# Kernel tuning notes

Hardware: AMD Instinct MI355X
Metric: run time of the kernel (lower is better)

Reference implementation:

```python
import jax, jax.numpy as jnp
import numpy as np

B, S, E, H, NF, NH, NIT = 64, 1024, 1024, 2048, 8, 4, 10
TEMP, XNOISE, LR = 1.0, 0.1, 0.1

PNAMES = ['ce_w1','ce_b1','ce_g','ce_be','ce_w2','ce_b2',
          'tp_w1','tp_b1','tp_g','tp_be','tp_w2','tp_b2',
          'en_w1','en_b1','en_g','en_be','en_w2','en_b2','en_w3','en_b3',
          'rn_w1','rn_b1','rn_g','rn_be','rn_w2','rn_b2']

def _ln(x, g, b):
    m = x.mean(-1, keepdims=True)
    v = ((x - m) ** 2).mean(-1, keepdims=True)
    return (x - m) * jax.lax.rsqrt(v + 1e-5) * g + b

def setup_inputs() -> dict:
    key = jax.random.key(0)
    ks = iter(jax.random.split(key, 40))
    w = lambda shape: jax.random.normal(next(ks), shape, jnp.float32) * 0.02
    z = lambda n: jnp.zeros((n,), jnp.float32)
    o = lambda n: jnp.ones((n,), jnp.float32)
    return {
        'current_embeddings': jax.random.normal(next(ks), (B, S, E), jnp.float32),
        'future_true': jax.random.normal(next(ks), (B, NF, E), jnp.float32),
        'ce_w1': w((E, H)), 'ce_b1': z(H), 'ce_g': o(H), 'ce_be': z(H), 'ce_w2': w((H, H)), 'ce_b2': z(H),
        'tp_w1': w((H, H)), 'tp_b1': z(H), 'tp_g': o(H), 'tp_be': z(H), 'tp_w2': w((H, E * NF)), 'tp_b2': z(E * NF),
        'en_w1': w((2 * E, H)), 'en_b1': z(H), 'en_g': o(H), 'en_be': z(H),
        'en_w2': w((H, H // 2)), 'en_b2': z(H // 2), 'en_w3': w((H // 2, 1)), 'en_b3': z(1),
        'rn_w1': w((3 * E, H)), 'rn_b1': z(H), 'rn_g': o(H), 'rn_be': z(H), 'rn_w2': w((H, E)), 'rn_b2': z(E),
    }

def _energy(emb, ce, ftrue, p):
    # emb: (..., NF, E); ce: (..., E); eval-mode (no dropout). Loop over t in
    # the original is a plain sum/NF -> vectorized over the NF axis here.
    ce_b = jnp.broadcast_to(ce[..., None, :], emb.shape)
    x = jnp.concatenate([emb, ce_b], axis=-1)            # (..., NF, 2E)
    x = jax.nn.relu(_ln(x @ p['en_w1'] + p['en_b1'], p['en_g'], p['en_be']))
    x = jax.nn.relu(x @ p['en_w2'] + p['en_b2'])
    coherence = (x @ p['en_w3'] + p['en_b3'])[..., 0].mean(-1)
    diffs = emb[..., 1:, :] - emb[..., :-1, :]
    smoothness = jnp.sqrt((diffs ** 2).sum(-1)).mean(-1)
    supervision = ((emb - ftrue) ** 2).mean((-1, -2))
    return coherence + 0.1 * smoothness + supervision

def _forward(cur, ft, p):
    ctx = cur.mean(1)                                    # (B, E)
    h = jax.nn.relu(_ln(ctx @ p['ce_w1'] + p['ce_b1'], p['ce_g'], p['ce_be']))
    ctx_h = h @ p['ce_w2'] + p['ce_b2']                  # (B, H)
    t = jax.nn.relu(_ln(ctx_h @ p['tp_w1'] + p['tp_b1'], p['tp_g'], p['tp_be']))
    traj = (t @ p['tp_w2'] + p['tp_b2']).reshape(B, 1, NF, E)
    # n_hypotheses identical deterministic trajectories + exploration noise
    noise = jax.random.normal(jax.random.key(42), (B, NH, NF, E), traj.dtype) * XNOISE
    hyp = traj + noise                                   # (B, NH, NF, E)
    ctx_e = ctx_h[:, :E]                                 # context[:, :embed_dim]

    emb = hyp.reshape(B * NH, NF, E)
    ce_flat = jnp.broadcast_to(ctx_e[:, None, :], (B, NH, E)).reshape(B * NH, E)
    ce_tiled = jnp.broadcast_to(ce_flat[:, None, :], (B * NH, NF, E))

    def refine(x, it):
        # all t-updates read the same snapshot of x -> fully vectorized over t
        prev = jnp.concatenate([x[:, :1], x[:, :-1]], axis=1)
        nxt = jnp.concatenate([x[:, 1:], x[:, -1:]], axis=1)
        neighbor = (prev + nxt) * 0.5
        inp = jnp.concatenate([x, ce_tiled, neighbor], axis=-1)   # (BH, NF, 3E)
        u = jax.nn.relu(_ln(inp @ p['rn_w1'] + p['rn_b1'], p['rn_g'], p['rn_be']))
        u = u @ p['rn_w2'] + p['rn_b2']
        x = x - LR * u
        ns = jax.random.normal(jax.random.fold_in(jax.random.key(7), it), x.shape, x.dtype) * (XNOISE * 0.1)
        x = jnp.where(it < NIT - 1, x + ns, x)  # noise on all but last iter
        return x, None

    emb, _ = jax.lax.scan(refine, emb, jnp.arange(NIT))
    refined = emb.reshape(B, NH, NF, E)

    ce_h = jnp.broadcast_to(ctx_e[:, None, :], (B, NH, E))
    ft_h = jnp.broadcast_to(ft[:, None], (B, NH, NF, E))
    energies = _energy(refined, ce_h, ft_h, p)           # (B, NH)
    probs = jax.nn.softmax(-energies / TEMP, axis=1)
    predictions = (refined * probs[..., None, None]).sum(1)  # (B, NF, E)
    return predictions

def reference(current_embeddings, future_true, ce_w1, ce_b1, ce_g, ce_be, ce_w2, ce_b2,
              tp_w1, tp_b1, tp_g, tp_be, tp_w2, tp_b2,
              en_w1, en_b1, en_g, en_be, en_w2, en_b2, en_w3, en_b3,
              rn_w1, rn_b1, rn_g, rn_be, rn_w2, rn_b2):
    p = dict(zip(PNAMES, (ce_w1, ce_b1, ce_g, ce_be, ce_w2, ce_b2,
                          tp_w1, tp_b1, tp_g, tp_be, tp_w2, tp_b2,
                          en_w1, en_b1, en_g, en_be, en_w2, en_b2, en_w3, en_b3,
                          rn_w1, rn_b1, rn_g, rn_be, rn_w2, rn_b2)))
    return _forward(current_embeddings, future_true, p)
```

## Files before the change

### kernel.cpp

```cpp
#include <hip/hip_runtime.h>
#include <hip/hip_bf16.h>
#include <stdint.h>

#define B_ 64
#define S_ 1024
#define E_ 1024
#define H_ 2048
#define NF_ 8
#define NH_ 4
#define NIT_ 10

typedef __attribute__((ext_vector_type(8))) short vshort8;
typedef __attribute__((ext_vector_type(8))) __bf16 vbf16x8;
typedef __attribute__((ext_vector_type(4))) float vfloat4;

typedef const __attribute__((address_space(1))) void* gas1_t;
typedef __attribute__((address_space(3))) void* las3_t;
__device__ __forceinline__ void gload16(const void* g, void* l) {
  __builtin_amdgcn_global_load_lds((gas1_t)g, (las3_t)l, 16, 0, 0);
}

__device__ __forceinline__ uint32_t rotl32(uint32_t v, int n) { return (v << n) | (v >> (32 - n)); }

__device__ __forceinline__ void threefry2x32(uint32_t k0, uint32_t k1, uint32_t x0, uint32_t x1,
                                             uint32_t& o0, uint32_t& o1) {
  uint32_t ks2 = k0 ^ k1 ^ 0x1BD11BDAu;
  x0 += k0; x1 += k1;
#define TF_R(r) { x0 += x1; x1 = rotl32(x1, (r)); x1 ^= x0; }
  TF_R(13) TF_R(15) TF_R(26) TF_R(6)
  x0 += k1;  x1 += ks2 + 1u;
  TF_R(17) TF_R(29) TF_R(16) TF_R(24)
  x0 += ks2; x1 += k0 + 2u;
  TF_R(13) TF_R(15) TF_R(26) TF_R(6)
  x0 += k0;  x1 += k1 + 3u;
  TF_R(17) TF_R(29) TF_R(16) TF_R(24)
  x0 += k1;  x1 += ks2 + 4u;
  TF_R(13) TF_R(15) TF_R(26) TF_R(6)
  x0 += ks2; x1 += k0 + 5u;
#undef TF_R
  o0 = x0; o1 = x1;
}

__device__ __forceinline__ uint32_t tf_bits_part(uint32_t k0, uint32_t k1, uint32_t i) {
  uint32_t o0, o1;
  threefry2x32(k0, k1, 0u, i, o0, o1);
  return o0 ^ o1;
}

__device__ __forceinline__ float erfinv_f(float x) {
  float w = -log1pf(-x * x);
  float p;
  if (w < 5.0f) {
    w -= 2.5f;
    p = 2.81022636e-08f;
    p = 3.43273939e-07f + p * w;
    p = -3.5233877e-06f + p * w;
    p = -4.39150654e-06f + p * w;
    p = 0.00021858087f + p * w;
    p = -0.00125372503f + p * w;
    p = -0.00417768164f + p * w;
    p = 0.246640727f + p * w;
    p = 1.50140941f + p * w;
  } else {
    w = sqrtf(w) - 3.0f;
    p = -0.000200214257f;
    p = 0.000100950558f + p * w;
    p = 0.00134934322f + p * w;
    p = -0.00367342844f + p * w;
    p = 0.00573950773f + p * w;
    p = -0.0076224613f + p * w;
    p = 0.00943887047f + p * w;
    p = 1.00167406f + p * w;
    p = 2.83297682f + p * w;
  }
  return p * x;
}

__device__ __forceinline__ float bits_to_normal(uint32_t bits) {
  uint32_t fb = (bits >> 9) | 0x3F800000u;
  float f = __uint_as_float(fb) - 1.0f;
  const float lo = -0.99999994f;
  float u = fmaxf(lo, f * 2.0f + lo);
  return 1.41421356f * erfinv_f(u);
}

__global__ __launch_bounds__(256) void colmean_partial(const float* __restrict__ cur,
                                                       float* __restrict__ part) {
  int blk = blockIdx.x;
  int b = blk >> 3, c = blk & 7;
  int t = threadIdx.x;
  const float* base = cur + ((size_t)b * S_ + (size_t)c * 128) * E_;
  float4 s = {0.f, 0.f, 0.f, 0.f};
  for (int si = 0; si < 128; ++si) {
    float4 v = *(const float4*)(base + (size_t)si * E_ + t * 4);
    s.x += v.x; s.y += v.y; s.z += v.z; s.w += v.w;
  }
  *(float4*)(part + ((size_t)c * B_ + b) * E_ + t * 4) = s;
}

__global__ __launch_bounds__(256) void colmean_final(const float* __restrict__ part,
                                                     float* __restrict__ ctx) {
  int i = blockIdx.x * 256 + threadIdx.x;
  float s = 0.f;
#pragma unroll
  for (int c = 0; c < 8; ++c) s += part[(size_t)c * (B_ * E_) + i];
  ctx[i] = s * (1.0f / S_);
}

__global__ __launch_bounds__(256) void cvt_bf16_v(const float* __restrict__ X,
                                                  __hip_bfloat16* __restrict__ Y) {
  int i = (blockIdx.x * 256 + threadIdx.x) * 8;
  float4 v0 = *(const float4*)(X + i);
  float4 v1 = *(const float4*)(X + i + 4);
  float v[8] = {v0.x, v0.y, v0.z, v0.w, v1.x, v1.y, v1.z, v1.w};
  __hip_bfloat16 o[8];
#pragma unroll
  for (int j = 0; j < 8; ++j) o[j] = __float2bfloat16(v[j]);
  *(vshort8*)&Y[i] = *(vshort8*)o;
}

__global__ __launch_bounds__(256) void transpose_to_bf16(const float* __restrict__ W,
                                                         __hip_bfloat16* __restrict__ Wt,
                                                         int K, int N, float scale) {
  __shared__ float tile[32][33];
  int n0 = blockIdx.x * 32, k0 = blockIdx.y * 32;
  int tx = threadIdx.x & 31, ty = threadIdx.x >> 5;
  for (int r = ty; r < 32; r += 8) tile[r][tx] = W[(size_t)(k0 + r) * N + n0 + tx];
  __syncthreads();
  for (int r = ty; r < 32; r += 8)
    Wt[(size_t)(n0 + r) * K + k0 + tx] = __float2bfloat16(tile[tx][r] * scale);
}

__global__ __launch_bounds__(256) void mfma_skinny(const __hip_bfloat16* __restrict__ A,
                                                   const __hip_bfloat16* __restrict__ Bt,
                                                   float* __restrict__ part,
                                                   int N, int K, int lda, int Kc) {
  __shared__ short AS[64 * 32];
  __shared__ short BS[128 * 32];
  int t = threadIdx.x;
  int lane = t & 63, wv = t >> 6;
  int n0 = blockIdx.x * 128;
  int kbeg = blockIdx.y * Kc;
  int wn = wv * 32;
  int lrow = lane & 15, kb = (lane >> 4) * 8;
  vfloat4 acc[4][2];
#pragma unroll
  for (int i = 0; i < 4; ++i)
#pragma unroll
    for (int j = 0; j < 2; ++j) acc[i][j] = (vfloat4){0.f, 0.f, 0.f, 0.f};
  const short* Ag = (const short*)A;
  const short* Bg = (const short*)Bt;
  int arow = lane >> 2;
  int acol = (lane & 3) * 8;
  for (int k0 = kbeg; k0 < kbeg + Kc; k0 += 32) {
    gload16(Ag + (size_t)(wv * 16 + arow) * lda + k0 + acol, &AS[(wv * 16) * 32]);
#pragma unroll
    for (int c = 0; c < 2; ++c)
      gload16(Bg + (size_t)(n0 + c * 64 + wv * 16 + arow) * K + k0 + acol,
              &BS[(c * 64 + wv * 16) * 32]);
    __syncthreads();
    vbf16x8 af[4], bq[2];
#pragma unroll
    for (int i = 0; i < 4; ++i) af[i] = *(const vbf16x8*)&AS[(i * 16 + lrow) * 32 + kb];
#pragma unroll
    for (int j = 0; j < 2; ++j) bq[j] = *(const vbf16x8*)&BS[(wn + j * 16 + lrow) * 32 + kb];
#pragma unroll
    for (int i = 0; i < 4; ++i)
#pragma unroll
      for (int j = 0; j < 2; ++j)
        acc[i][j] = __builtin_amdgcn_mfma_f32_16x16x32_bf16(af[i], bq[j], acc[i][j], 0, 0, 0);
    __syncthreads();
  }
  size_t zbase = (size_t)blockIdx.y * 64;
  int crow0 = (lane >> 4) * 4;
  int ccol0 = n0 + wn + lrow;
#pragma unroll
  for (int i = 0; i < 4; ++i) {
#pragma unroll
    for (int j = 0; j < 2; ++j) {
      int col = ccol0 + j * 16;
#pragma unroll
      for (int r = 0; r < 4; ++r) {
        int rowi = i * 16 + crow0 + r;
        part[(zbase + rowi) * N + col] = acc[i][j][r];
      }
    }
  }
}

template <bool BF16OUT>
__global__ __launch_bounds__(256) void reduce_bias(const float* __restrict__ part,
                                                   const float* __restrict__ bias,
                                                   float* __restrict__ C,
                                                   __hip_bfloat16* __restrict__ Cb,
                                                   int N, int SK) {
  int i = blockIdx.x * 256 + threadIdx.x;
  int col = i & (N - 1);
  float s = bias[col];
  for (int z = 0; z < SK; ++z) s += part[(size_t)z * 64 * N + i];
  C[i] = s;
  if (BF16OUT) Cb[i] = __float2bfloat16(s);
}

__global__ __launch_bounds__(256) void ln2048red(const float* __restrict__ part,
                                                 const float* __restrict__ bias,
                                                 const float* __restrict__ g,
                                                 const float* __restrict__ be,
                                                 __hip_bfloat16* __restrict__ out, int SK) {
  __shared__ float red[256];
  int row = blockIdx.x, t = threadIdx.x;
  int j0 = t * 8;
  float v[8];
  *(float4*)&v[0] = *(const float4*)(bias + j0);
  *(float4*)&v[4] = *(const float4*)(bias + j0 + 4);
  for (int z = 0; z < SK; ++z) {
    const float* p = part + (size_t)z * 64 * 2048 + (size_t)row * 2048 + j0;
    float4 a0 = *(const float4*)p, a1 = *(const float4*)(p + 4);
    v[0] += a0.x; v[1] += a0.y; v[2] += a0.z; v[3] += a0.w;
    v[4] += a1.x; v[5] += a1.y; v[6] += a1.z; v[7] += a1.w;
  }
  float s = 0.f;
#pragma unroll
  for (int j = 0; j < 8; ++j) s += v[j];
  red[t] = s; __syncthreads();
  for (int k = 128; k > 0; k >>= 1) { if (t < k) red[t] += red[t + k]; __syncthreads(); }
  float mean = red[0] * (1.0f / 2048.0f);
  __syncthreads();
  float s2 = 0.f;
#pragma unroll
  for (int j = 0; j < 8; ++j) { float d = v[j] - mean; s2 += d * d; }
  red[t] = s2; __syncthreads();
  for (int k = 128; k > 0; k >>= 1) { if (t < k) red[t] += red[t + k]; __syncthreads(); }
  float rstd = rsqrtf(red[0] * (1.0f / 2048.0f) + 1e-5f);
  __hip_bfloat16 o[8];
#pragma unroll
  for (int j = 0; j < 8; ++j) {
    float y = (v[j] - mean) * rstd * g[j0 + j] + be[j0 + j];
    o[j] = __float2bfloat16(fmaxf(y, 0.f));
  }
  *(vshort8*)&out[(size_t)row * 2048 + j0] = *(vshort8*)o;
}

template <int NEIGH>
__global__ __launch_bounds__(256) void ln_comb(const float* __restrict__ G,
                                               const float* __restrict__ cterm,
                                               const float* __restrict__ g,
                                               const float* __restrict__ be,
                                               __hip_bfloat16* __restrict__ out) {
  __shared__ float red[256];
  int row = blockIdx.x, t = threadIdx.x;
  int j0 = t * 8;
  const int GS = NEIGH ? 4096 : 2048;
  float v[8];
  {
    const float* p = G + (size_t)row * GS + j0;
    float4 a0 = *(const float4*)p, a1 = *(const float4*)(p + 4);
    v[0] = a0.x; v[1] = a0.y; v[2] = a0.z; v[3] = a0.w;
    v[4] = a1.x; v[5] = a1.y; v[6] = a1.z; v[7] = a1.w;
  }
  {
    const float* p = cterm + (size_t)(row >> 5) * 2048 + j0;
    float4 a0 = *(const float4*)p, a1 = *(const float4*)(p + 4);
    v[0] += a0.x; v[1] += a0.y; v[2] += a0.z; v[3] += a0.w;
    v[4] += a1.x; v[5] += a1.y; v[6] += a1.z; v[7] += a1.w;
  }
  if (NEIGH) {
    int f = row & 7;
    int prow = (f == 0) ? row : row - 1;
    int nrow = (f == NF_ - 1) ? row : row + 1;
    const float* pp = G + (size_t)prow * 4096 + 2048 + j0;
    const float* pn = G + (size_t)nrow * 4096 + 2048 + j0;
    float4 a0 = *(const float4*)pp, a1 = *(const float4*)(pp + 4);
    float4 b0 = *(const float4*)pn, b1 = *(const float4*)(pn + 4);
    v[0] += a0.x + b0.x; v[1] += a0.y + b0.y; v[2] += a0.z + b0.z; v[3] += a0.w + b0.w;
    v[4] += a1.x + b1.x; v[5] += a1.y + b1.y; v[6] += a1.z + b1.z; v[7] += a1.w + b1.w;
  }
  float s = 0.f;
#pragma unroll
  for (int j = 0; j < 8; ++j) s += v[j];
  red[t] = s; __syncthreads();
  for (int k = 128; k > 0; k >>= 1) { if (t < k) red[t] += red[t + k]; __syncthreads(); }
  float mean = red[0] * (1.0f / 2048.0f);
  __syncthreads();
  float s2 = 0.f;
#pragma unroll
  for (int j = 0; j < 8; ++j) { float d = v[j] - mean; s2 += d * d; }
  red[t] = s2; __syncthreads();
  for (int k = 128; k > 0; k >>= 1) { if (t < k) red[t] += red[t + k]; __syncthreads(); }
  float rstd = rsqrtf(red[0] * (1.0f / 2048.0f) + 1e-5f);
  __hip_bfloat16 o[8];
#pragma unroll
  for (int j = 0; j < 8; ++j) {
    float y = (v[j] - mean) * rstd * g[j0 + j] + be[j0 + j];
    o[j] = __float2bfloat16(fmaxf(y, 0.f));
  }
  *(vshort8*)&out[(size_t)row * 2048 + j0] = *(vshort8*)o;
}

template <int MODE>
__global__ __launch_bounds__(256) void gemm_gl(const __hip_bfloat16* __restrict__ A,
                                               const __hip_bfloat16* __restrict__ Bt,
                                               const float* __restrict__ bias,
                                               float* __restrict__ Cout,
                                               __hip_bfloat16* __restrict__ Cbout,
                                               int M, int N, int K, int it) {
  __shared__ short Als[128 * 64];
  __shared__ short Bls[64 * 64];
  int t = threadIdx.x;
  int lane = t & 63, wv = t >> 6;
  int n0 = blockIdx.x * 64, m0 = blockIdx.y * 128;
  int wm = (wv >> 1) * 64, wn = (wv & 1) * 32;
  int lrow = lane & 15, kb = (lane >> 4) * 8;
  vfloat4 acc[4][2];
#pragma unroll
  for (int i = 0; i < 4; ++i)
#pragma unroll
    for (int j = 0; j < 2; ++j) acc[i][j] = (vfloat4){0.f, 0.f, 0.f, 0.f};
  const short* Ag = (const short*)A;
  const short* Bg = (const short*)Bt;
  int arow = lane >> 3;
  int acol = (lane & 7) * 8;
  for (int k0 = 0; k0 < K; k0 += 64) {
#pragma unroll
    for (int c = 0; c < 4; ++c)
      gload16(Ag + (size_t)(m0 + c * 32 + wv * 8 + arow) * K + k0 + acol,
              &Als[(c * 32 + wv * 8) * 64]);
#pragma unroll
    for (int c = 0; c < 2; ++c)
      gload16(Bg + (size_t)(n0 + c * 32 + wv * 8 + arow) * K + k0 + acol,
              &Bls[(c * 32 + wv * 8) * 64]);
    __syncthreads();
    vbf16x8 af[2][4], bq[2][2];
#pragma unroll
    for (int ks = 0; ks < 2; ++ks) {
#pragma unroll
      for (int i = 0; i < 4; ++i)
        af[ks][i] = *(const vbf16x8*)&Als[(wm + i * 16 + lrow) * 64 + ks * 32 + kb];
#pragma unroll
      for (int j = 0; j < 2; ++j)
        bq[ks][j] = *(const vbf16x8*)&Bls[(wn + j * 16 + lrow) * 64 + ks * 32 + kb];
    }
#pragma unroll
    for (int ks = 0; ks < 2; ++ks)
#pragma unroll
      for (int i = 0; i < 4; ++i)
#pragma unroll
        for (int j = 0; j < 2; ++j)
          acc[i][j] = __builtin_amdgcn_mfma_f32_16x16x32_bf16(af[ks][i], bq[ks][j], acc[i][j], 0, 0, 0);
    __syncthreads();
  }
  int crow0 = m0 + wm + (lane >> 4) * 4;
  int ccol0 = n0 + wn + lrow;
  if (MODE == 2) {
    uint32_t key0 = 0, key1 = 0;
    bool addn = (it < NIT_ - 1);
    if (addn) threefry2x32(0u, 7u, 0u, (uint32_t)it, key0, key1);
#pragma unroll
    for (int i = 0; i < 4; ++i) {
#pragma unroll
      for (int j = 0; j < 2; ++j) {
        int col = ccol0 + j * 16;
        float bv = bias[col];
#pragma unroll
        for (int r = 0; r < 4; ++r) {
          uint32_t idx = (uint32_t)(crow0 + i * 16 + r) * N + col;
          float xv = Cout[idx] - 0.1f * (acc[i][j][r] + bv);
          if (addn) xv += 0.01f * bits_to_normal(tf_bits_part(key0, key1, idx));
          Cout[idx] = xv;
          Cbout[idx] = __float2bfloat16(xv);
        }
      }
    }
  } else {
#pragma unroll
    for (int i = 0; i < 4; ++i) {
#pragma unroll
      for (int j = 0; j < 2; ++j) {
        int col = ccol0 + j * 16;
        float bv = (MODE == 3) ? 0.f : bias[col];
#pragma unroll
        for (int r = 0; r < 4; ++r) {
          float v = acc[i][j][r] + bv;
          if (MODE == 1) v = fmaxf(v, 0.f);
          Cout[(size_t)(crow0 + i * 16 + r) * N + col] = v;
        }
      }
    }
  }
}

__global__ __launch_bounds__(256) void reduce_traj_noise(const float* __restrict__ part,
                                                         const float* __restrict__ bias,
                                                         float* __restrict__ x,
                                                         __hip_bfloat16* __restrict__ xb,
                                                         int SK) {
  int i = blockIdx.x * 256 + threadIdx.x;
  int fe = i & 8191;
  float s = bias[fe];
  for (int z = 0; z < SK; ++z) s += part[(size_t)z * 524288 + i];
  int b = i >> 13;
#pragma unroll
  for (int h = 0; h < NH_; ++h) {
    uint32_t xi = (uint32_t)(b * 32768 + h * 8192 + fe);
    float xv = s + 0.1f * bits_to_normal(tf_bits_part(0u, 42u, xi));
    x[xi] = xv;
    xb[xi] = __float2bfloat16(xv);
  }
}

__global__ __launch_bounds__(256) void rowdot(const float* __restrict__ X2,
                                              const float* __restrict__ w3,
                                              const float* __restrict__ b3,
                                              float* __restrict__ srow) {
  __shared__ float red[256];
  int row = blockIdx.x, t = threadIdx.x;
  const float* xr = X2 + (size_t)row * E_;
  float s = 0.f;
  for (int c = t; c < E_; c += 256) s += xr[c] * w3[c];
  red[t] = s; __syncthreads();
  for (int k = 128; k > 0; k >>= 1) { if (t < k) red[t] += red[t + k]; __syncthreads(); }
  if (t == 0) srow[row] = red[0] + b3[0];
}

__global__ __launch_bounds__(256) void energy_final(const float* __restrict__ x,
                                                    const float* __restrict__ ft,
                                                    const float* __restrict__ srow,
                                                    float* __restrict__ energ) {
  __shared__ float red[256];
  int bh = blockIdx.x, t = threadIdx.x;
  int b = bh >> 2;
  const float* xb = x + (size_t)bh * (NF_ * E_);
  const float* fb = ft + (size_t)b * (NF_ * E_);
  float sup = 0.f;
  for (int i = t; i < NF_ * E_; i += 256) { float d = xb[i] - fb[i]; sup += d * d; }
  red[t] = sup; __syncthreads();
  for (int k = 128; k > 0; k >>= 1) { if (t < k) red[t] += red[t + k]; __syncthreads(); }
  float supervision = red[0] / (NF_ * E_);
  float smooth = 0.f;
  for (int d = 0; d < NF_ - 1; ++d) {
    __syncthreads();
    float sd = 0.f;
    for (int e = t; e < E_; e += 256) {
      float df = xb[(d + 1) * E_ + e] - xb[d * E_ + e];
      sd += df * df;
    }
    red[t] = sd; __syncthreads();
    for (int k = 128; k > 0; k >>= 1) { if (t < k) red[t] += red[t + k]; __syncthreads(); }
    smooth += sqrtf(red[0]);
  }
  smooth *= (1.0f / (NF_ - 1));
  if (t == 0) {
    float coh = 0.f;
    for (int f = 0; f < NF_; ++f) coh += srow[bh * NF_ + f];
    coh *= (1.0f / NF_);
    energ[bh] = coh + 0.1f * smooth + supervision;
  }
}

__global__ void softmax_probs(const float* __restrict__ energ, float* __restrict__ probs) {
  int b = threadIdx.x;
  if (b < B_) {
    float e[NH_], m = -1e30f;
#pragma unroll
    for (int h = 0; h < NH_; ++h) { e[h] = -energ[b * NH_ + h]; m = fmaxf(m, e[h]); }
    float s = 0.f, p[NH_];
#pragma unroll
    for (int h = 0; h < NH_; ++h) { p[h] = expf(e[h] - m); s += p[h]; }
#pragma unroll
    for (int h = 0; h < NH_; ++h) probs[b * NH_ + h] = p[h] / s;
  }
}

__global__ __launch_bounds__(256) void predict(const float* __restrict__ x,
                                               const float* __restrict__ probs,
                                               float* __restrict__ out) {
  int i = blockIdx.x * 256 + threadIdx.x;
  int b = i >> 13, fe = i & 8191;
  float s = 0.f;
#pragma unroll
  for (int h = 0; h < NH_; ++h) s += x[(size_t)(b * NH_ + h) * 8192 + fe] * probs[b * NH_ + h];
  out[i] = s;
}

extern "C" void kernel_launch(void* const* d_in, const int* in_sizes, int n_in,
                              void* d_out, int out_size, void* d_ws, size_t ws_size,
                              hipStream_t stream) {
  const float* cur   = (const float*)d_in[0];
  const float* ftrue = (const float*)d_in[1];
  const float* ce_w1 = (const float*)d_in[2];
  const float* ce_b1 = (const float*)d_in[3];
  const float* ce_g  = (const float*)d_in[4];
  const float* ce_be = (const float*)d_in[5];
  const float* ce_w2 = (const float*)d_in[6];
  const float* ce_b2 = (const float*)d_in[7];
  const float* tp_w1 = (const float*)d_in[8];
  const float* tp_b1 = (const float*)d_in[9];
  const float* tp_g  = (const float*)d_in[10];
  const float* tp_be = (const float*)d_in[11];
  const float* tp_w2 = (const float*)d_in[12];
  const float* tp_b2 = (const float*)d_in[13];
  const float* en_w1 = (const float*)d_in[14];
  const float* en_b1 = (const float*)d_in[15];
  const float* en_g  = (const float*)d_in[16];
  const float* en_be = (const float*)d_in[17];
  const float* en_w2 = (const float*)d_in[18];
  const float* en_b2 = (const float*)d_in[19];
  const float* en_w3 = (const float*)d_in[20];
  const float* en_b3 = (const float*)d_in[21];
  const float* rn_w1 = (const float*)d_in[22];
  const float* rn_b1 = (const float*)d_in[23];
  const float* rn_g  = (const float*)d_in[24];
  const float* rn_be = (const float*)d_in[25];
  const float* rn_w2 = (const float*)d_in[26];
  const float* rn_b2 = (const float*)d_in[27];
  (void)in_sizes; (void)n_in; (void)out_size; (void)ws_size;

  char* w = (char*)d_ws;
  size_t off = 0;
  auto alloc = [&](size_t bytes) -> void* {
    void* p = w + off;
    off += (bytes + 255) & ~(size_t)255;
    return p;
  };
  float* part   = (float*)alloc((size_t)8 * B_ * E_ * 4);
  float* ctx    = (float*)alloc((size_t)B_ * E_ * 4);
  float* g1     = (float*)alloc((size_t)B_ * H_ * 4);
  float* x      = (float*)alloc((size_t)2097152 * 4);
  float* skpart = (float*)alloc((size_t)8 * 64 * 8192 * 4);
  float* G      = (float*)alloc((size_t)2048 * 4096 * 4);
  float* u      = (float*)alloc((size_t)2048 * 1024 * 4);
  __hip_bfloat16* ub   = (__hip_bfloat16*)alloc((size_t)2048 * 2048 * 2);
  __hip_bfloat16* x_b  = (__hip_bfloat16*)alloc((size_t)2048 * 1024 * 2);
  float* srow   = (float*)alloc((size_t)2048 * 4);
  float* energ  = (float*)alloc((size_t)256 * 4);
  float* probs  = (float*)alloc((size_t)256 * 4);
  float* cterm  = (float*)alloc((size_t)B_ * H_ * 4);
  float* ecterm = (float*)alloc((size_t)B_ * H_ * 4);
  __hip_bfloat16* Wcat_t = (__hip_bfloat16*)alloc((size_t)4096 * 1024 * 2);
  __hip_bfloat16* Wb_t   = (__hip_bfloat16*)alloc((size_t)2048 * 1024 * 2);
  __hip_bfloat16* rn_w2t = (__hip_bfloat16*)alloc((size_t)1024 * 2048 * 2);
  __hip_bfloat16* en1a_t = (__hip_bfloat16*)alloc((size_t)2048 * 1024 * 2);
  __hip_bfloat16* en1b_t = (__hip_bfloat16*)alloc((size_t)2048 * 1024 * 2);
  __hip_bfloat16* en_w2t = (__hip_bfloat16*)alloc((size_t)1024 * 2048 * 2);
  __hip_bfloat16* ctx_b  = (__hip_bfloat16*)alloc((size_t)B_ * E_ * 2);
  __hip_bfloat16* ctxh_b = (__hip_bfloat16*)alloc((size_t)B_ * H_ * 2);
  __hip_bfloat16* lnb    = (__hip_bfloat16*)alloc((size_t)B_ * H_ * 2);
  __hip_bfloat16* cw1t = (__hip_bfloat16*)alloc((size_t)2048 * 1024 * 2);
  __hip_bfloat16* cw2t = (__hip_bfloat16*)alloc((size_t)2048 * 2048 * 2);
  __hip_bfloat16* tw1t = (__hip_bfloat16*)alloc((size_t)2048 * 2048 * 2);
  __hip_bfloat16* tw2t = (__hip_bfloat16*)alloc((size_t)8192 * 2048 * 2);

  colmean_partial<<<512, 256, 0, stream>>>(cur, part);
  colmean_final<<<256, 256, 0, stream>>>(part, ctx);

  transpose_to_bf16<<<dim3(64, 32), 256, 0, stream>>>(rn_w1, Wcat_t, 1024, 2048, 1.0f);
  transpose_to_bf16<<<dim3(64, 32), 256, 0, stream>>>(rn_w1 + (size_t)2048 * 2048,
                                                      Wcat_t + (size_t)2048 * 1024, 1024, 2048, 0.5f);
  transpose_to_bf16<<<dim3(64, 32), 256, 0, stream>>>(rn_w1 + (size_t)1024 * 2048, Wb_t, 1024, 2048, 1.0f);
  transpose_to_bf16<<<dim3(32, 64), 256, 0, stream>>>(rn_w2, rn_w2t, 2048, 1024, 1.0f);
  transpose_to_bf16<<<dim3(64, 32), 256, 0, stream>>>(en_w1, en1a_t, 1024, 2048, 1.0f);
  transpose_to_bf16<<<dim3(64, 32), 256, 0, stream>>>(en_w1 + (size_t)1024 * 2048, en1b_t, 1024, 2048, 1.0f);
  transpose_to_bf16<<<dim3(32, 64), 256, 0, stream>>>(en_w2, en_w2t, 2048, 1024, 1.0f);
  transpose_to_bf16<<<dim3(64, 32), 256, 0, stream>>>(ce_w1, cw1t, 1024, 2048, 1.0f);
  transpose_to_bf16<<<dim3(64, 64), 256, 0, stream>>>(ce_w2, cw2t, 2048, 2048, 1.0f);
  transpose_to_bf16<<<dim3(64, 64), 256, 0, stream>>>(tp_w1, tw1t, 2048, 2048, 1.0f);
  transpose_to_bf16<<<dim3(256, 64), 256, 0, stream>>>(tp_w2, tw2t, 2048, 8192, 1.0f);

  cvt_bf16_v<<<32, 256, 0, stream>>>(ctx, ctx_b);
  mfma_skinny<<<dim3(16, 4), 256, 0, stream>>>(ctx_b, cw1t, skpart, 2048, 1024, 1024, 256);
  ln2048red<<<B_, 256, 0, stream>>>(skpart, ce_b1, ce_g, ce_be, lnb, 4);
  mfma_skinny<<<dim3(16, 8), 256, 0, stream>>>(lnb, cw2t, skpart, 2048, 2048, 2048, 256);
  reduce_bias<true><<<512, 256, 0, stream>>>(skpart, ce_b2, g1, ctxh_b, 2048, 8);
  mfma_skinny<<<dim3(16, 8), 256, 0, stream>>>(ctxh_b, tw1t, skpart, 2048, 2048, 2048, 256);
  ln2048red<<<B_, 256, 0, stream>>>(skpart, tp_b1, tp_g, tp_be, lnb, 8);
  mfma_skinny<<<dim3(64, 8), 256, 0, stream>>>(lnb, tw2t, skpart, 8192, 2048, 2048, 256);
  reduce_traj_noise<<<2048, 256, 0, stream>>>(skpart, tp_b2, x, x_b, 8);

  mfma_skinny<<<dim3(16, 4), 256, 0, stream>>>(ctxh_b, Wb_t, skpart, 2048, 1024, 2048, 256);
  reduce_bias<false><<<512, 256, 0, stream>>>(skpart, rn_b1, cterm, nullptr, 2048, 4);
  mfma_skinny<<<dim3(16, 4), 256, 0, stream>>>(ctxh_b, en1b_t, skpart, 2048, 1024, 2048, 256);
  reduce_bias<false><<<512, 256, 0, stream>>>(skpart, en_b1, ecterm, nullptr, 2048, 4);

  for (int it = 0; it < NIT_; ++it) {
    gemm_gl<3><<<dim3(64, 16), 256, 0, stream>>>(x_b, Wcat_t, nullptr, G, nullptr,
                                                 2048, 4096, 1024, 0);
    ln_comb<1><<<2048, 256, 0, stream>>>(G, cterm, rn_g, rn_be, ub);
    gemm_gl<2><<<dim3(16, 16), 256, 0, stream>>>(ub, rn_w2t, rn_b2, x, x_b,
                                                 2048, 1024, 2048, it);
  }

  gemm_gl<3><<<dim3(32, 16), 256, 0, stream>>>(x_b, en1a_t, nullptr, G, nullptr,
                                               2048, 2048, 1024, 0);
  ln_comb<0><<<2048, 256, 0, stream>>>(G, ecterm, en_g, en_be, ub);
  gemm_gl<1><<<dim3(16, 16), 256, 0, stream>>>(ub, en_w2t, en_b2, u, nullptr,
                                               2048, 1024, 2048, 0);
  rowdot<<<2048, 256, 0, stream>>>(u, en_w3, en_b3, srow);
  energy_final<<<256, 256, 0, stream>>>(x, ftrue, srow, energ);
  softmax_probs<<<1, 64, 0, stream>>>(energ, probs);
  predict<<<2048, 256, 0, stream>>>(x, probs, (float*)d_out);
}
```

Before: 1.353 ms.

## Store refine GEMM output in bf16 with new 128x128 GEMM; merge cterm GEMMs

Adds a new 128x128-tile bf16 MFMA GEMM that writes its output directly as bf16, and makes ln_comb read that bf16 buffer instead of fp32. This halves the write and read traffic of the large per-iteration intermediate. The two context-term skinny GEMMs and their bias reductions are also merged into one wider GEMM plus a combined reduction. The cost is reduced precision on the pre-LayerNorm activations. The MODE==3 bias guard in gemm_gl is also removed, which is harmless now that mode 3 is no longer launched.

Result: slower. 1.490 ms (+10.1%).

```diff
diff --git a/kernel.cpp b/kernel.cpp
--- a/kernel.cpp
+++ b/kernel.cpp
@@ -84,6 +84,15 @@
   return 1.41421356f * erfinv_f(u);
 }
 
+__device__ __forceinline__ void load_bf8(const __hip_bfloat16* p, float v[8]) {
+  vshort8 s = *(const vshort8*)p;
+#pragma unroll
+  for (int j = 0; j < 8; ++j) {
+    uint32_t b = ((uint32_t)(uint16_t)s[j]) << 16;
+    v[j] = __uint_as_float(b);
+  }
+}
+
 __global__ __launch_bounds__(256) void colmean_partial(const float* __restrict__ cur,
                                                        float* __restrict__ part) {
   int blk = blockIdx.x;
@@ -200,6 +209,17 @@
   for (int z = 0; z < SK; ++z) s += part[(size_t)z * 64 * N + i];
   C[i] = s;
   if (BF16OUT) Cb[i] = __float2bfloat16(s);
+}
+
+__global__ __launch_bounds__(256) void reduce_cterm(const float* __restrict__ part,
+                                                    const float* __restrict__ rn_b1,
+                                                    const float* __restrict__ en_b1,
+                                                    float* __restrict__ out, int SK) {
+  int i = blockIdx.x * 256 + threadIdx.x;
+  int col = i & 4095;
+  float s = (col < 2048) ? rn_b1[col] : en_b1[col - 2048];
+  for (int z = 0; z < SK; ++z) s += part[(size_t)z * 64 * 4096 + i];
+  out[i] = s;
 }
 
 __global__ __launch_bounds__(256) void ln2048red(const float* __restrict__ part,
@@ -242,8 +262,8 @@
 }
 
 template <int NEIGH>
-__global__ __launch_bounds__(256) void ln_comb(const float* __restrict__ G,
-                                               const float* __restrict__ cterm,
+__global__ __launch_bounds__(256) void ln_comb(const __hip_bfloat16* __restrict__ G,
+                                               const float* __restrict__ cterm, int cstride,
                                                const float* __restrict__ g,
                                                const float* __restrict__ be,
                                                __hip_bfloat16* __restrict__ out) {
@@ -252,14 +272,9 @@
   int j0 = t * 8;
   const int GS = NEIGH ? 4096 : 2048;
   float v[8];
+  load_bf8(G + (size_t)row * GS + j0, v);
   {
-    const float* p = G + (size_t)row * GS + j0;
-    float4 a0 = *(const float4*)p, a1 = *(const float4*)(p + 4);
-    v[0] = a0.x; v[1] = a0.y; v[2] = a0.z; v[3] = a0.w;
-    v[4] = a1.x; v[5] = a1.y; v[6] = a1.z; v[7] = a1.w;
-  }
-  {
-    const float* p = cterm + (size_t)(row >> 5) * 2048 + j0;
+    const float* p = cterm + (size_t)(row >> 5) * cstride + j0;
     float4 a0 = *(const float4*)p, a1 = *(const float4*)(p + 4);
     v[0] += a0.x; v[1] += a0.y; v[2] += a0.z; v[3] += a0.w;
     v[4] += a1.x; v[5] += a1.y; v[6] += a1.z; v[7] += a1.w;
@@ -268,12 +283,11 @@
     int f = row & 7;
     int prow = (f == 0) ? row : row - 1;
     int nrow = (f == NF_ - 1) ? row : row + 1;
-    const float* pp = G + (size_t)prow * 4096 + 2048 + j0;
-    const float* pn = G + (size_t)nrow * 4096 + 2048 + j0;
-    float4 a0 = *(const float4*)pp, a1 = *(const float4*)(pp + 4);
-    float4 b0 = *(const float4*)pn, b1 = *(const float4*)(pn + 4);
-    v[0] += a0.x + b0.x; v[1] += a0.y + b0.y; v[2] += a0.z + b0.z; v[3] += a0.w + b0.w;
-    v[4] += a1.x + b1.x; v[5] += a1.y + b1.y; v[6] += a1.z + b1.z; v[7] += a1.w + b1.w;
+    float a[8], b[8];
+    load_bf8(G + (size_t)prow * 4096 + 2048 + j0, a);
+    load_bf8(G + (size_t)nrow * 4096 + 2048 + j0, b);
+#pragma unroll
+    for (int j = 0; j < 8; ++j) v[j] += a[j] + b[j];
   }
   float s = 0.f;
 #pragma unroll
@@ -295,6 +309,61 @@
     o[j] = __float2bfloat16(fmaxf(y, 0.f));
   }
   *(vshort8*)&out[(size_t)row * 2048 + j0] = *(vshort8*)o;
+}
+
+__global__ __launch_bounds__(256) void gemm_bf(const __hip_bfloat16* __restrict__ A,
+                                               const __hip_bfloat16* __restrict__ Bt,
+                                               __hip_bfloat16* __restrict__ Cb,
+                                               int M, int N, int K) {
+  __shared__ short Als[128 * 32];
+  __shared__ short Bls[128 * 32];
+  int t = threadIdx.x;
+  int lane = t & 63, wv = t >> 6;
+  int n0 = blockIdx.x * 128, m0 = blockIdx.y * 128;
+  int wm = (wv >> 1) * 64, wn = (wv & 1) * 64;
+  int lrow = lane & 15, kb = (lane >> 4) * 8;
+  vfloat4 acc[4][4];
+#pragma unroll
+  for (int i = 0; i < 4; ++i)
+#pragma unroll
+    for (int j = 0; j < 4; ++j) acc[i][j] = (vfloat4){0.f, 0.f, 0.f, 0.f};
+  const short* Ag = (const short*)A;
+  const short* Bg = (const short*)Bt;
+  int arow = lane >> 2;
+  int acol = (lane & 3) * 8;
+  for (int k0 = 0; k0 < K; k0 += 32) {
+#pragma unroll
+    for (int c = 0; c < 2; ++c) {
+      gload16(Ag + (size_t)(m0 + c * 64 + wv * 16 + arow) * K + k0 + acol,
+              &Als[(c * 64 + wv * 16) * 32]);
+      gload16(Bg + (size_t)(n0 + c * 64 + wv * 16 + arow) * K + k0 + acol,
+              &Bls[(c * 64 + wv * 16) * 32]);
+    }
+    __syncthreads();
+    vbf16x8 af[4], bq[4];
+#pragma unroll
+    for (int i = 0; i < 4; ++i) af[i] = *(const vbf16x8*)&Als[(wm + i * 16 + lrow) * 32 + kb];
+#pragma unroll
+    for (int j = 0; j < 4; ++j) bq[j] = *(const vbf16x8*)&Bls[(wn + j * 16 + lrow) * 32 + kb];
+#pragma unroll
+    for (int i = 0; i < 4; ++i)
+#pragma unroll
+      for (int j = 0; j < 4; ++j)
+        acc[i][j] = __builtin_amdgcn_mfma_f32_16x16x32_bf16(af[i], bq[j], acc[i][j], 0, 0, 0);
+    __syncthreads();
+  }
+  int crow0 = m0 + wm + (lane >> 4) * 4;
+  int ccol0 = n0 + wn + lrow;
+#pragma unroll
+  for (int i = 0; i < 4; ++i) {
+#pragma unroll
+    for (int j = 0; j < 4; ++j) {
+      int col = ccol0 + j * 16;
+#pragma unroll
+      for (int r = 0; r < 4; ++r)
+        Cb[(size_t)(crow0 + i * 16 + r) * N + col] = __float2bfloat16(acc[i][j][r]);
+    }
+  }
 }
 
 template <int MODE>
@@ -377,7 +446,7 @@
 #pragma unroll
       for (int j = 0; j < 2; ++j) {
         int col = ccol0 + j * 16;
-        float bv = (MODE == 3) ? 0.f : bias[col];
+        float bv = bias[col];
 #pragma unroll
         for (int r = 0; r < 4; ++r) {
           float v = acc[i][j][r] + bv;
@@ -527,20 +596,18 @@
   float* g1     = (float*)alloc((size_t)B_ * H_ * 4);
   float* x      = (float*)alloc((size_t)2097152 * 4);
   float* skpart = (float*)alloc((size_t)8 * 64 * 8192 * 4);
-  float* G      = (float*)alloc((size_t)2048 * 4096 * 4);
+  __hip_bfloat16* Gb = (__hip_bfloat16*)alloc((size_t)2048 * 4096 * 2);
   float* u      = (float*)alloc((size_t)2048 * 1024 * 4);
   __hip_bfloat16* ub   = (__hip_bfloat16*)alloc((size_t)2048 * 2048 * 2);
   __hip_bfloat16* x_b  = (__hip_bfloat16*)alloc((size_t)2048 * 1024 * 2);
   float* srow   = (float*)alloc((size_t)2048 * 4);
   float* energ  = (float*)alloc((size_t)256 * 4);
   float* probs  = (float*)alloc((size_t)256 * 4);
-  float* cterm  = (float*)alloc((size_t)B_ * H_ * 4);
-  float* ecterm = (float*)alloc((size_t)B_ * H_ * 4);
-  __hip_bfloat16* Wcat_t = (__hip_bfloat16*)alloc((size_t)4096 * 1024 * 2);
-  __hip_bfloat16* Wb_t   = (__hip_bfloat16*)alloc((size_t)2048 * 1024 * 2);
+  float* ctermcat = (float*)alloc((size_t)B_ * 4096 * 4);
+  __hip_bfloat16* Wcat_t  = (__hip_bfloat16*)alloc((size_t)4096 * 1024 * 2);
+  __hip_bfloat16* Wbcat_t = (__hip_bfloat16*)alloc((size_t)4096 * 1024 * 2);
   __hip_bfloat16* rn_w2t = (__hip_bfloat16*)alloc((size_t)1024 * 2048 * 2);
   __hip_bfloat16* en1a_t = (__hip_bfloat16*)alloc((size_t)2048 * 1024 * 2);
-  __hip_bfloat16* en1b_t = (__hip_bfloat16*)alloc((size_t)2048 * 1024 * 2);
   __hip_bfloat16* en_w2t = (__hip_bfloat16*)alloc((size_t)1024 * 2048 * 2);
   __hip_bfloat16* ctx_b  = (__hip_bfloat16*)alloc((size_t)B_ * E_ * 2);
   __hip_bfloat16* ctxh_b = (__hip_bfloat16*)alloc((size_t)B_ * H_ * 2);
@@ -556,10 +623,11 @@
   transpose_to_bf16<<<dim3(64, 32), 256, 0, stream>>>(rn_w1, Wcat_t, 1024, 2048, 1.0f);
   transpose_to_bf16<<<dim3(64, 32), 256, 0, stream>>>(rn_w1 + (size_t)2048 * 2048,
                                                       Wcat_t + (size_t)2048 * 1024, 1024, 2048, 0.5f);
-  transpose_to_bf16<<<dim3(64, 32), 256, 0, stream>>>(rn_w1 + (size_t)1024 * 2048, Wb_t, 1024, 2048, 1.0f);
+  transpose_to_bf16<<<dim3(64, 32), 256, 0, stream>>>(rn_w1 + (size_t)1024 * 2048, Wbcat_t, 1024, 2048, 1.0f);
+  transpose_to_bf16<<<dim3(64, 32), 256, 0, stream>>>(en_w1 + (size_t)1024 * 2048,
+                                                      Wbcat_t + (size_t)2048 * 1024, 1024, 2048, 1.0f);
   transpose_to_bf16<<<dim3(32, 64), 256, 0, stream>>>(rn_w2, rn_w2t, 2048, 1024, 1.0f);
   transpose_to_bf16<<<dim3(64, 32), 256, 0, stream>>>(en_w1, en1a_t, 1024, 2048, 1.0f);
-  transpose_to_bf16<<<dim3(64, 32), 256, 0, stream>>>(en_w1 + (size_t)1024 * 2048, en1b_t, 1024, 2048, 1.0f);
   transpose_to_bf16<<<dim3(32, 64), 256, 0, stream>>>(en_w2, en_w2t, 2048, 1024, 1.0f);
   transpose_to_bf16<<<dim3(64, 32), 256, 0, stream>>>(ce_w1, cw1t, 1024, 2048, 1.0f);
   transpose_to_bf16<<<dim3(64, 64), 256, 0, stream>>>(ce_w2, cw2t, 2048, 2048, 1.0f);
@@ -576,22 +644,18 @@
   mfma_skinny<<<dim3(64, 8), 256, 0, stream>>>(lnb, tw2t, skpart, 8192, 2048, 2048, 256);
   reduce_traj_noise<<<2048, 256, 0, stream>>>(skpart, tp_b2, x, x_b, 8);
 
-  mfma_skinny<<<dim3(16, 4), 256, 0, stream>>>(ctxh_b, Wb_t, skpart, 2048, 1024, 2048, 256);
-  reduce_bias<false><<<512, 256, 0, stream>>>(skpart, rn_b1, cterm, nullptr, 2048, 4);
-  mfma_skinny<<<dim3(16, 4), 256, 0, stream>>>(ctxh_b, en1b_t, skpart, 2048, 1024, 2048, 256);
-  reduce_bias<false><<<512, 256, 0, stream>>>(skpart, en_b1, ecterm, nullptr, 2048, 4);
+  mfma_skinny<<<dim3(32, 4), 256, 0, stream>>>(ctxh_b, Wbcat_t, skpart, 4096, 1024, 2048, 256);
+  reduce_cterm<<<1024, 256, 0, stream>>>(skpart, rn_b1, en_b1, ctermcat, 4);
 
   for (int it = 0; it < NIT_; ++it) {
-    gemm_gl<3><<<dim3(64, 16), 256, 0, stream>>>(x_b, Wcat_t, nullptr, G, nullptr,
-                                                 2048, 4096, 1024, 0);
-    ln_comb<1><<<2048, 256, 0, stream>>>(G, cterm, rn_g, rn_be, ub);
+    gemm_bf<<<dim3(32, 16), 256, 0, stream>>>(x_b, Wcat_t, Gb, 2048, 4096, 1024);
+    ln_comb<1><<<2048, 256, 0, stream>>>(Gb, ctermcat, 4096, rn_g, rn_be, ub);
     gemm_gl<2><<<dim3(16, 16), 256, 0, stream>>>(ub, rn_w2t, rn_b2, x, x_b,
                                                  2048, 1024, 2048, it);
   }
 
-  gemm_gl<3><<<dim3(32, 16), 256, 0, stream>>>(x_b, en1a_t, nullptr, G, nullptr,
-                                               2048, 2048, 1024, 0);
-  ln_comb<0><<<2048, 256, 0, stream>>>(G, ecterm, en_g, en_be, ub);
+  gemm_bf<<<dim3(16, 16), 256, 0, stream>>>(x_b, en1a_t, Gb, 2048, 2048, 1024);
+  ln_comb<0><<<2048, 256, 0, stream>>>(Gb, ctermcat + 2048, 4096, en_g, en_be, ub);
   gemm_gl<1><<<dim3(16, 16), 256, 0, stream>>>(ub, en_w2t, en_b2, u, nullptr,
                                                2048, 1024, 2048, 0);
   rowdot<<<2048, 256, 0, stream>>>(u, en_w3, en_b3, srow);
```
